# Kernel tuning notes

Hardware: AMD Instinct MI355X
Metric: run time of the kernel (lower is better)

## Reference

```python
import jax, jax.numpy as jnp
import numpy as np


def setup_inputs() -> dict:
    key = jax.random.key(0)
    k1, k2 = jax.random.split(key)
    preds = jax.random.normal(k1, (16, 4096, 3), dtype=jnp.float32)
    gts = jax.random.normal(k2, (16, 4096, 3), dtype=jnp.float32)
    return {"preds": preds, "gts": gts}


def _pairwise_sqdist(x, y):
    # x: [B, N1, D], y: [B, N2, D] -> P: [B, N1, N2]
    rx = jnp.sum(x * x, axis=-1)  # [B, N1]
    ry = jnp.sum(y * y, axis=-1)  # [B, N2]
    zz = jnp.einsum("bnd,bmd->bnm", x, y)  # [B, N1, N2]
    return rx[:, :, None] + ry[:, None, :] - 2.0 * zz


def reference(preds, gts):
    # Symmetric Hausdorff distance (squared-dist version) per batch element.
    P = _pairwise_sqdist(preds, gts)  # [B, N1, N2]
    # min over preds (axis 1) for each gt point, then max over gt points
    loss1 = jnp.max(jnp.min(P, axis=1), axis=1)  # [B]
    # min over gts (axis 2) for each pred point, then max over pred points
    loss2 = jnp.max(jnp.min(P, axis=2), axis=1)  # [B]
    return (loss1 + loss2) * 0.5
```

## Files before the change

### kernel.cpp

```cpp
#include <hip/hip_runtime.h>
#include <math.h>


#define NPTS 4096
#define NB 16
#define TPB 256
#define WAVES 4
#define HPW 32
#define HPB (WAVES * HPW)
#define NHB (NPTS / HPB)
#define SPLIT 4
#define OPP (NPTS / SPLIT)
#define TILES (OPP / 32)

#define WSMIN_N (2 * NB * NPTS)

typedef _Float16 h8 __attribute__((ext_vector_type(8)));
typedef float f16v __attribute__((ext_vector_type(16)));

__global__ __launch_bounds__(TPB) void haus_scan_kernel(
        const float* __restrict__ preds, const float* __restrict__ gts,
        unsigned int* __restrict__ wsmin) {
    const int hb  = blockIdx.x & (NHB - 1);
    const int sp  = blockIdx.x >> 5;
    const int b   = blockIdx.y;
    const int dir = blockIdx.z;
    const int t   = threadIdx.x;
    const int lane = t & 63, w = t >> 6;
    const int l31 = lane & 31, half = lane >> 5;

    const float* home = (dir == 0) ? gts : preds;
    const float* opp  = (dir == 0) ? preds : gts;
    const float* hbp = home + (size_t)b * NPTS * 3;
    const float* obp = opp  + (size_t)b * NPTS * 3;

    __shared__ h8 srec[2 * OPP];
    __shared__ float shg[WAVES][HPW];

    for (int i = 0; i < OPP / TPB; ++i) {
        int p = i * TPB + t;
        const float* s = obp + (size_t)(sp * OPP + p) * 3;
        float x = s[0], y = s[1], z = s[2];
        float hp = fmaf(x, x, fmaf(y, y, z * z));
        _Float16 xh = (_Float16)x, yh = (_Float16)y, zh = (_Float16)z;
        _Float16 xl = (_Float16)(x - (float)xh);
        _Float16 yl = (_Float16)(y - (float)yh);
        _Float16 zl = (_Float16)(z - (float)zh);
        _Float16 hph = (_Float16)hp, hpl = (_Float16)(hp - (float)hph);
        h8 lo, hi;
        lo[0] = xh; lo[1] = yh; lo[2] = zh;
        lo[3] = xl; lo[4] = yl; lo[5] = zl;
        lo[6] = xh; lo[7] = yh;
        hi[0] = zh;
        hi[1] = hph; hi[2] = hpl;
        hi[3] = (_Float16)0; hi[4] = (_Float16)0;
        hi[5] = (_Float16)0; hi[6] = (_Float16)0; hi[7] = (_Float16)0;
        srec[p] = lo;
        srec[OPP + p] = hi;
    }

    int m = hb * HPB + w * HPW + l31;
    float gx = hbp[m * 3 + 0], gy = hbp[m * 3 + 1], gz = hbp[m * 3 + 2];
    float hg = fmaf(gx, gx, fmaf(gy, gy, gz * gz));
    shg[w][l31] = hg;
    _Float16 gxh = (_Float16)gx, gyh = (_Float16)gy, gzh = (_Float16)gz;
    _Float16 gxl = (_Float16)(gx - (float)gxh);
    _Float16 gyl = (_Float16)(gy - (float)gyh);
    _Float16 gzl = (_Float16)(gz - (float)gzh);
    const _Float16 n2 = (_Float16)(-2.0f);
    h8 afrag;
    if (half == 0) {
        afrag[0] = n2 * gxh; afrag[1] = n2 * gyh; afrag[2] = n2 * gzh;
        afrag[3] = n2 * gxh; afrag[4] = n2 * gyh; afrag[5] = n2 * gzh;
        afrag[6] = n2 * gxl; afrag[7] = n2 * gyl;
    } else {
        afrag[0] = n2 * gzl;
        afrag[1] = (_Float16)1; afrag[2] = (_Float16)1;
        afrag[3] = (_Float16)0; afrag[4] = (_Float16)0;
        afrag[5] = (_Float16)0; afrag[6] = (_Float16)0; afrag[7] = (_Float16)0;
    }

    f16v zc = {};
    float best[16];
#pragma unroll
    for (int r = 0; r < 16; ++r) best[r] = INFINITY;

    __syncthreads();

    const int base = half * OPP + l31;
#pragma unroll 2
    for (int tt = 0; tt < TILES; ++tt) {
        h8 bfrag = srec[base + tt * 32];
        f16v D = __builtin_amdgcn_mfma_f32_32x32x16_f16(afrag, bfrag, zc, 0, 0, 0);
#pragma unroll
        for (int r = 0; r < 16; ++r) best[r] = fminf(best[r], D[r]);
    }

#pragma unroll
    for (int off = 16; off >= 1; off >>= 1) {
#pragma unroll
        for (int r = 0; r < 16; ++r)
            best[r] = fminf(best[r], __shfl_xor(best[r], off, 64));
    }

    unsigned int* slot = wsmin + ((size_t)dir * NB + b) * NPTS + hb * HPB + w * HPW;
    if (l31 == 0) {
#pragma unroll
        for (int r = 0; r < 16; ++r) {
            int row = (r & 3) + 8 * (r >> 2) + 4 * half;
            float d = best[r] + shg[w][row];
            d = fmaxf(d, 0.0f);
            atomicMin(slot + row, __float_as_uint(d));
        }
    }
}

__global__ __launch_bounds__(TPB) void haus_final_kernel(
        const unsigned int* __restrict__ wsmin, float* __restrict__ out) {
    const int b = blockIdx.x;
    const int t = threadIdx.x;
    const float4* w0 = (const float4*)(wsmin + ((size_t)0 * NB + b) * NPTS);
    const float4* w1 = (const float4*)(wsmin + ((size_t)1 * NB + b) * NPTS);
    float m1 = -INFINITY, m2 = -INFINITY;
#pragma unroll
    for (int r = 0; r < NPTS / 4 / TPB; ++r) {
        float4 a = w0[r * TPB + t];
        float4 c = w1[r * TPB + t];
        m1 = fmaxf(fmaxf(fmaxf(a.x, a.y), fmaxf(a.z, a.w)), m1);
        m2 = fmaxf(fmaxf(fmaxf(c.x, c.y), fmaxf(c.z, c.w)), m2);
    }
#pragma unroll
    for (int off = 32; off > 0; off >>= 1) {
        m1 = fmaxf(m1, __shfl_down(m1, off, 64));
        m2 = fmaxf(m2, __shfl_down(m2, off, 64));
    }
    __shared__ float s1[4], s2[4];
    if ((t & 63) == 0) { s1[t >> 6] = m1; s2[t >> 6] = m2; }
    __syncthreads();
    if (t == 0) {
        float a = fmaxf(fmaxf(s1[0], s1[1]), fmaxf(s1[2], s1[3]));
        float c = fmaxf(fmaxf(s2[0], s2[1]), fmaxf(s2[2], s2[3]));
        out[b] = 0.5f * (a + c);
    }
}

extern "C" void kernel_launch(void* const* d_in, const int* in_sizes, int n_in,
                              void* d_out, int out_size, void* d_ws, size_t ws_size,
                              hipStream_t stream) {
    const float* preds = (const float*)d_in[0];
    const float* gts   = (const float*)d_in[1];
    float* out = (float*)d_out;
    unsigned int* wsmin = (unsigned int*)d_ws;

    hipMemsetAsync(wsmin, 0xFF, (size_t)WSMIN_N * sizeof(unsigned int), stream);

    haus_scan_kernel<<<dim3(NHB * SPLIT, NB, 2), dim3(TPB), 0, stream>>>(
        preds, gts, wsmin);

    haus_final_kernel<<<dim3(NB), dim3(TPB), 0, stream>>>(wsmin, out);
}
```

Measured before the change: 93.30 us.

## Process two home-point tiles per wave to reuse each B fragment twice

Each wave now handles 64 home points with two A fragments, issuing two MFMAs per shared-memory B fragment load, and the opposite set is split 8 ways instead of 4. This halves LDS B-fragment loads per MFMA and halves the per-block staging of the opposite set, keeping the grid size the same. It doubles the accumulator registers (32 min values), which may reduce occupancy, and doubles the shuffle reduction and atomics per lane.

Result: slower. 105.8 us (+13.4%).

```diff
diff --git a/kernel.cpp b/kernel.cpp
--- a/kernel.cpp
+++ b/kernel.cpp
@@ -6,10 +6,10 @@
 #define NB 16
 #define TPB 256
 #define WAVES 4
-#define HPW 32
+#define HPW 64
 #define HPB (WAVES * HPW)
 #define NHB (NPTS / HPB)
-#define SPLIT 4
+#define SPLIT 8
 #define OPP (NPTS / SPLIT)
 #define TILES (OPP / 32)
 
@@ -22,7 +22,7 @@
         const float* __restrict__ preds, const float* __restrict__ gts,
         unsigned int* __restrict__ wsmin) {
     const int hb  = blockIdx.x & (NHB - 1);
-    const int sp  = blockIdx.x >> 5;
+    const int sp  = blockIdx.x >> 4;
     const int b   = blockIdx.y;
     const int dir = blockIdx.z;
     const int t   = threadIdx.x;
@@ -59,31 +59,38 @@
         srec[OPP + p] = hi;
     }
 
-    int m = hb * HPB + w * HPW + l31;
-    float gx = hbp[m * 3 + 0], gy = hbp[m * 3 + 1], gz = hbp[m * 3 + 2];
-    float hg = fmaf(gx, gx, fmaf(gy, gy, gz * gz));
-    shg[w][l31] = hg;
-    _Float16 gxh = (_Float16)gx, gyh = (_Float16)gy, gzh = (_Float16)gz;
-    _Float16 gxl = (_Float16)(gx - (float)gxh);
-    _Float16 gyl = (_Float16)(gy - (float)gyh);
-    _Float16 gzl = (_Float16)(gz - (float)gzh);
-    const _Float16 n2 = (_Float16)(-2.0f);
-    h8 afrag;
-    if (half == 0) {
-        afrag[0] = n2 * gxh; afrag[1] = n2 * gyh; afrag[2] = n2 * gzh;
-        afrag[3] = n2 * gxh; afrag[4] = n2 * gyh; afrag[5] = n2 * gzh;
-        afrag[6] = n2 * gxl; afrag[7] = n2 * gyl;
-    } else {
-        afrag[0] = n2 * gzl;
-        afrag[1] = (_Float16)1; afrag[2] = (_Float16)1;
-        afrag[3] = (_Float16)0; afrag[4] = (_Float16)0;
-        afrag[5] = (_Float16)0; afrag[6] = (_Float16)0; afrag[7] = (_Float16)0;
+    h8 afrag[2];
+    {
+#pragma unroll
+        for (int a = 0; a < 2; ++a) {
+            int m = hb * HPB + w * HPW + a * 32 + l31;
+            float gx = hbp[m * 3 + 0], gy = hbp[m * 3 + 1], gz = hbp[m * 3 + 2];
+            float hg = fmaf(gx, gx, fmaf(gy, gy, gz * gz));
+            shg[w][a * 32 + l31] = hg;
+            _Float16 gxh = (_Float16)gx, gyh = (_Float16)gy, gzh = (_Float16)gz;
+            _Float16 gxl = (_Float16)(gx - (float)gxh);
+            _Float16 gyl = (_Float16)(gy - (float)gyh);
+            _Float16 gzl = (_Float16)(gz - (float)gzh);
+            const _Float16 n2 = (_Float16)(-2.0f);
+            h8 f;
+            if (half == 0) {
+                f[0] = n2 * gxh; f[1] = n2 * gyh; f[2] = n2 * gzh;
+                f[3] = n2 * gxh; f[4] = n2 * gyh; f[5] = n2 * gzh;
+                f[6] = n2 * gxl; f[7] = n2 * gyl;
+            } else {
+                f[0] = n2 * gzl;
+                f[1] = (_Float16)1; f[2] = (_Float16)1;
+                f[3] = (_Float16)0; f[4] = (_Float16)0;
+                f[5] = (_Float16)0; f[6] = (_Float16)0; f[7] = (_Float16)0;
+            }
+            afrag[a] = f;
+        }
     }
 
     f16v zc = {};
-    float best[16];
+    float best0[16], best1[16];
 #pragma unroll
-    for (int r = 0; r < 16; ++r) best[r] = INFINITY;
+    for (int r = 0; r < 16; ++r) { best0[r] = INFINITY; best1[r] = INFINITY; }
 
     __syncthreads();
 
@@ -91,16 +98,21 @@
 #pragma unroll 2
     for (int tt = 0; tt < TILES; ++tt) {
         h8 bfrag = srec[base + tt * 32];
-        f16v D = __builtin_amdgcn_mfma_f32_32x32x16_f16(afrag, bfrag, zc, 0, 0, 0);
+        f16v D0 = __builtin_amdgcn_mfma_f32_32x32x16_f16(afrag[0], bfrag, zc, 0, 0, 0);
+        f16v D1 = __builtin_amdgcn_mfma_f32_32x32x16_f16(afrag[1], bfrag, zc, 0, 0, 0);
 #pragma unroll
-        for (int r = 0; r < 16; ++r) best[r] = fminf(best[r], D[r]);
+        for (int r = 0; r < 16; ++r) best0[r] = fminf(best0[r], D0[r]);
+#pragma unroll
+        for (int r = 0; r < 16; ++r) best1[r] = fminf(best1[r], D1[r]);
     }
 
 #pragma unroll
     for (int off = 16; off >= 1; off >>= 1) {
 #pragma unroll
-        for (int r = 0; r < 16; ++r)
-            best[r] = fminf(best[r], __shfl_xor(best[r], off, 64));
+        for (int r = 0; r < 16; ++r) {
+            best0[r] = fminf(best0[r], __shfl_xor(best0[r], off, 64));
+            best1[r] = fminf(best1[r], __shfl_xor(best1[r], off, 64));
+        }
     }
 
     unsigned int* slot = wsmin + ((size_t)dir * NB + b) * NPTS + hb * HPB + w * HPW;
@@ -108,9 +120,10 @@
 #pragma unroll
         for (int r = 0; r < 16; ++r) {
             int row = (r & 3) + 8 * (r >> 2) + 4 * half;
-            float d = best[r] + shg[w][row];
-            d = fmaxf(d, 0.0f);
-            atomicMin(slot + row, __float_as_uint(d));
+            float d0 = fmaxf(best0[r] + shg[w][row], 0.0f);
+            float d1 = fmaxf(best1[r] + shg[w][32 + row], 0.0f);
+            atomicMin(slot + row, __float_as_uint(d0));
+            atomicMin(slot + 32 + row, __float_as_uint(d1));
         }
     }
 }
```
